# Kernel tuning notes

Measured on AMD Instinct MI355X. Metric: run time of the kernel, lower is better.

The kernel has to match this reference:

```python
import jax, jax.numpy as jnp
import numpy as np

IN_FEATURES = 1024
OUT_FEATURES = 512
TAU_U = 20.0
DT = 1.0


def setup_inputs() -> dict:
    key = jax.random.key(0)
    k_x, k_w = jax.random.split(key)
    B, T = 32, 1024
    x = jax.random.normal(k_x, (B, T, IN_FEATURES), dtype=jnp.float32)
    # uniform(-sqrt(1/in), sqrt(1/in)) as in reset_parameters
    bound = float(np.sqrt(1.0 / IN_FEATURES))
    weight = jax.random.uniform(k_w, (OUT_FEATURES, IN_FEATURES), dtype=jnp.float32,
                                minval=-bound, maxval=bound)
    bias = jnp.zeros((OUT_FEATURES,), dtype=jnp.float32)
    # fixed tau trainer: decay = exp(-dt / tau), tau fixed at 20
    decay_u = jnp.full((OUT_FEATURES,), float(np.exp(-DT / TAU_U)), dtype=jnp.float32)
    return {"x": x, "weight": weight, "bias": bias, "decay_u": decay_u}


def reference(x, weight, bias, decay_u):
    # x: [B, T, in] -> current: [B, T, out] (one big GEMM instead of T small ones)
    current = jnp.einsum("bti,oi->bto", x, weight) + bias
    B = x.shape[0]
    u0 = jnp.zeros((B, OUT_FEATURES), dtype=x.dtype)

    drive = (1.0 - decay_u) * current          # [B, T, out]
    drive_t = jnp.swapaxes(drive, 0, 1)        # [T, B, out] for scan

    def step(u_tm1, d_t):
        u_t = decay_u * u_tm1 + d_t
        return u_t, u_t

    _, outs_t = jax.lax.scan(step, u0, drive_t)  # [T, B, out]
    outputs = jnp.swapaxes(outs_t, 0, 1)          # [B, T, out]
    # states: stack([u0, u1, ..., uT], dim=1).unsqueeze(0) -> [1, B, T+1, out]
    states = jnp.concatenate([u0[:, None, :], outputs], axis=1)[None]
    return outputs, states
```

## Files before the change

### kernel.cpp

```cpp
#include <hip/hip_runtime.h>
#include <hip/hip_bf16.h>
#include <stdint.h>

#define BATCH 32
#define SEQT  1024
#define INF   1024
#define OUTF  512
#define MROWS (BATCH * SEQT)

typedef __attribute__((ext_vector_type(8))) short short8;
typedef __attribute__((ext_vector_type(4))) short s16x4;
typedef __attribute__((ext_vector_type(4))) float f32x4;

__device__ __forceinline__ short f2bf(float f) {
    return (short)__builtin_bit_cast(unsigned short, __float2bfloat16(f));
}

__device__ __forceinline__ void gll16(const short* g, short* l) {
    __builtin_amdgcn_global_load_lds(
        (const __attribute__((address_space(1))) unsigned int*)g,
        (__attribute__((address_space(3))) unsigned int*)l, 16, 0, 0);
}

__global__ __launch_bounds__(256) void wcvt_kernel(
    const float* __restrict__ W, short* __restrict__ Wb) {
    const int i = (blockIdx.x * 256 + threadIdx.x) << 3;
    const f32x4 a = *(const f32x4*)&W[i];
    const f32x4 b = *(const f32x4*)&W[i + 4];
    short8 h;
#pragma unroll
    for (int q = 0; q < 4; ++q) { h[q] = f2bf(a[q]); h[4 + q] = f2bf(b[q]); }
    *(short8*)&Wb[i] = h;
}

__global__ __launch_bounds__(256) void scanx_kernel(
    const float* __restrict__ X, const float* __restrict__ decay,
    short* __restrict__ Xs, float* __restrict__ states) {
    const int gid = blockIdx.x * 256 + threadIdx.x;
    const int k4  = gid & 255;
    const int seg = (gid >> 8) & 7;
    const int b   = gid >> 11;

    const float d   = decay[0];
    const float omd = 1.0f - d;
    const float* xb = X  + (size_t)b * SEQT * INF + (k4 << 2);
    short*       ob = Xs + (size_t)b * SEQT * INF + (k4 << 2);

    if (seg == 0 && k4 < 128) {
        f32x4 z = {0.f, 0.f, 0.f, 0.f};
        *(f32x4*)&states[(size_t)b * ((SEQT + 1) * OUTF) + (k4 << 2)] = z;
    }

    f32x4 u = {0.f, 0.f, 0.f, 0.f};
    const int t0 = seg << 7;
    const int tw = (seg == 0) ? 0 : (t0 - 128);
    for (int t = tw; t < t0; t += 8) {
        f32x4 r[8];
#pragma unroll
        for (int j = 0; j < 8; ++j) r[j] = *(const f32x4*)&xb[(size_t)(t + j) * INF];
#pragma unroll
        for (int j = 0; j < 8; ++j)
#pragma unroll
            for (int q = 0; q < 4; ++q) u[q] = fmaf(d, u[q], omd * r[j][q]);
    }
    for (int t = t0; t < t0 + 128; t += 8) {
        f32x4 r[8];
#pragma unroll
        for (int j = 0; j < 8; ++j) r[j] = *(const f32x4*)&xb[(size_t)(t + j) * INF];
#pragma unroll
        for (int j = 0; j < 8; ++j) {
            s16x4 h;
#pragma unroll
            for (int q = 0; q < 4; ++q) { u[q] = fmaf(d, u[q], omd * r[j][q]); h[q] = f2bf(u[q]); }
            *(s16x4*)&ob[(size_t)(t + j) * INF] = h;
        }
    }
}

__global__ __launch_bounds__(512, 1) void gemm_bf16_kernel(
    const short* __restrict__ Xs, const short* __restrict__ Wb,
    const float* __restrict__ bias, const float* __restrict__ decay,
    float* __restrict__ outp, float* __restrict__ states, const int writeOut) {
    __shared__ short lds_s[65536];

    const int tid = threadIdx.x;
    const int bid = blockIdx.x;
    const int xcd = bid & 7;
    const int ii  = bid >> 3;
    const int mt  = (xcd << 4) + (ii >> 1);
    const int nt  = ii & 1;
    const int m0 = mt << 8;
    const int o0 = nt << 8;

    const int wv   = tid >> 6;
    const int lane = tid & 63;
    const int wr = wv >> 1;
    const int wc = wv & 1;
    const int r0 = lane & 15;
    const int lg = lane >> 4;

    const short* sA[4];
    const short* sB[4];
    int dG[4];
#pragma unroll
    for (int j = 0; j < 4; ++j) {
        const int gf  = (j << 9) + tid;
        const int row = gf >> 3;
        const int ss  = (gf & 7) ^ (row & 7);
        sA[j] = Xs + (size_t)(m0 + row) * INF + (ss << 3);
        sB[j] = Wb + (size_t)(o0 + row) * INF + (ss << 3);
        dG[j] = gf << 3;
    }

#define STAGE(BUF, KB)                                                       \
    {                                                                        \
        short* a_ = &lds_s[(BUF) << 15];                                     \
        short* b_ = a_ + 16384;                                              \
        _Pragma("unroll")                                                    \
        for (int j = 0; j < 4; ++j) gll16(sA[j] + (KB), &a_[dG[j]]);         \
        _Pragma("unroll")                                                    \
        for (int j = 0; j < 4; ++j) gll16(sB[j] + (KB), &b_[dG[j]]);         \
    }

    f32x4 acc[4][8] = {};

    STAGE(0, 0)
    __syncthreads();

    for (int kt = 0; kt < 16; ++kt) {
        if (kt < 15) STAGE((kt + 1) & 1, (kt + 1) << 6);
        const short* la = &lds_s[(kt & 1) << 15];
        const short* lb = la + 16384;
#pragma unroll
        for (int kk = 0; kk < 2; ++kk) {
            short8 av[4], bv[8];
#pragma unroll
            for (int mi = 0; mi < 4; ++mi) {
                const int row = (wr << 6) + (mi << 4) + r0;
                const int g   = (kk << 2) + lg;
                av[mi] = *(const short8*)&la[(row << 6) + ((g ^ (row & 7)) << 3)];
            }
#pragma unroll
            for (int ni = 0; ni < 8; ++ni) {
                const int row = (wc << 7) + (ni << 4) + r0;
                const int g   = (kk << 2) + lg;
                bv[ni] = *(const short8*)&lb[(row << 6) + ((g ^ (row & 7)) << 3)];
            }
            __builtin_amdgcn_s_setprio(1);
#pragma unroll
            for (int mi = 0; mi < 4; ++mi)
#pragma unroll
                for (int ni = 0; ni < 8; ++ni)
                    acc[mi][ni] = __builtin_amdgcn_mfma_f32_16x16x32_bf16(
                        av[mi], bv[ni], acc[mi][ni], 0, 0, 0);
            __builtin_amdgcn_s_setprio(0);
        }
        __syncthreads();
    }
#undef STAGE

    float* csf = (float*)lds_s;
    const float l2d = log2f(decay[0]);
    const int b = m0 >> 10;
#pragma unroll
    for (int p = 0; p < 4; ++p) {
        if (wr == p) {
#pragma unroll
            for (int ni = 0; ni < 8; ++ni) {
                const int col = (wc << 7) + (ni << 4) + r0;
#pragma unroll
                for (int mi = 0; mi < 4; ++mi) {
                    const int lr = (mi << 4) + (lg << 2);
#pragma unroll
                    for (int j = 0; j < 4; ++j)
                        csf[(lr + j) * 260 + col] = acc[mi][ni][j];
                }
            }
        }
        __syncthreads();
#pragma unroll
        for (int it = 0; it < 8; ++it) {
            const int idx = (it << 9) + tid;
            const int row = idx >> 6;
            const int c4  = idx & 63;
            f32x4 v = *(const f32x4*)&csf[row * 260 + (c4 << 2)];
            const int m = m0 + (p << 6) + row;
            const int t = m & (SEQT - 1);
            const float coef = 1.0f - exp2f(l2d * (float)(t + 1));
            const f32x4 bb = *(const f32x4*)&bias[o0 + (c4 << 2)];
#pragma unroll
            for (int q = 0; q < 4; ++q) v[q] = fmaf(bb[q], coef, v[q]);
            const size_t oaddr = (size_t)m * OUTF + o0 + (c4 << 2);
            if (writeOut) *(f32x4*)&outp[oaddr] = v;
            *(f32x4*)&states[oaddr + (size_t)(b + 1) * OUTF] = v;
        }
        if (p < 3) __syncthreads();
    }
}

__global__ __launch_bounds__(256) void copy_out_kernel(
    float* __restrict__ outp, const float* __restrict__ states) {
    const size_t total = (size_t)MROWS * OUTF / 4;
    size_t i = (size_t)blockIdx.x * 256 + threadIdx.x;
    const size_t stride = (size_t)gridDim.x * 256;
    for (; i < total; i += stride) {
        const size_t b = i >> 17;
        *(f32x4*)&outp[i << 2] = *(const f32x4*)&states[(i << 2) + (b + 1) * OUTF];
    }
}

extern "C" void kernel_launch(void* const* d_in, const int* in_sizes, int n_in,
                              void* d_out, int out_size, void* d_ws, size_t ws_size,
                              hipStream_t stream) {
    const float* x     = (const float*)d_in[0];
    const float* w     = (const float*)d_in[1];
    const float* bias  = (const float*)d_in[2];
    const float* decay = (const float*)d_in[3];

    float* outp   = (float*)d_out;
    float* states = outp + (size_t)MROWS * OUTF;

    const size_t xs_shorts = (size_t)MROWS * INF;
    const size_t need = (xs_shorts + (size_t)OUTF * INF) * 2;
    const bool primary = (ws_size >= need);

    short* xs  = primary ? (short*)d_ws : (short*)outp;
    short* wbf = primary ? ((short*)d_ws + xs_shorts) : (short*)d_ws;

    wcvt_kernel<<<dim3((OUTF * INF) / (256 * 8)), dim3(256), 0, stream>>>(w, wbf);
    scanx_kernel<<<dim3(256), dim3(256), 0, stream>>>(x, decay, xs, states);
    gemm_bf16_kernel<<<dim3(256), dim3(512), 0, stream>>>(
        xs, wbf, bias, decay, outp, states, primary ? 1 : 0);
    if (!primary)
        copy_out_kernel<<<dim3(2048), dim3(256), 0, stream>>>(outp, states);
}
```

Before: 108.6 us.

## Double-buffer input scan loads and halve per-thread width to double threads

The input-side decay scan now has each thread handle two features instead of four, which doubles the grid from 256 to 512 blocks. Each thread loads 16 timesteps at a time into two register buffers that alternate, so the loads for the next burst are issued while the current burst is scanned. Scheduling barriers keep the compiler from interleaving the two phases. The aim is more memory-level parallelism in this bandwidth-bound pre-pass, at the cost of narrower 8-byte loads and 4-byte stores and more registers per thread.

```diff
diff --git a/kernel.cpp b/kernel.cpp
--- a/kernel.cpp
+++ b/kernel.cpp
@@ -9,7 +9,8 @@
 #define MROWS (BATCH * SEQT)
 
 typedef __attribute__((ext_vector_type(8))) short short8;
-typedef __attribute__((ext_vector_type(4))) short s16x4;
+typedef __attribute__((ext_vector_type(2))) short s16x2;
+typedef __attribute__((ext_vector_type(2))) float f32x2;
 typedef __attribute__((ext_vector_type(4))) float f32x4;
 
 __device__ __forceinline__ short f2bf(float f) {
@@ -37,44 +38,60 @@
     const float* __restrict__ X, const float* __restrict__ decay,
     short* __restrict__ Xs, float* __restrict__ states) {
     const int gid = blockIdx.x * 256 + threadIdx.x;
-    const int k4  = gid & 255;
-    const int seg = (gid >> 8) & 7;
-    const int b   = gid >> 11;
+    const int k2  = gid & 511;
+    const int seg = (gid >> 9) & 7;
+    const int b   = gid >> 12;
 
     const float d   = decay[0];
     const float omd = 1.0f - d;
-    const float* xb = X  + (size_t)b * SEQT * INF + (k4 << 2);
-    short*       ob = Xs + (size_t)b * SEQT * INF + (k4 << 2);
-
-    if (seg == 0 && k4 < 128) {
-        f32x4 z = {0.f, 0.f, 0.f, 0.f};
-        *(f32x4*)&states[(size_t)b * ((SEQT + 1) * OUTF) + (k4 << 2)] = z;
-    }
-
-    f32x4 u = {0.f, 0.f, 0.f, 0.f};
+    const float* xb = X  + (size_t)b * SEQT * INF + (k2 << 1);
+    short*       ob = Xs + (size_t)b * SEQT * INF + (k2 << 1);
+
+    if (seg == 0 && k2 < 256) {
+        f32x2 z = {0.f, 0.f};
+        *(f32x2*)&states[(size_t)b * ((SEQT + 1) * OUTF) + (k2 << 1)] = z;
+    }
+
+    float u0 = 0.f, u1 = 0.f;
     const int t0 = seg << 7;
     const int tw = (seg == 0) ? 0 : (t0 - 128);
-    for (int t = tw; t < t0; t += 8) {
-        f32x4 r[8];
-#pragma unroll
-        for (int j = 0; j < 8; ++j) r[j] = *(const f32x4*)&xb[(size_t)(t + j) * INF];
-#pragma unroll
-        for (int j = 0; j < 8; ++j)
-#pragma unroll
-            for (int q = 0; q < 4; ++q) u[q] = fmaf(d, u[q], omd * r[j][q]);
-    }
-    for (int t = t0; t < t0 + 128; t += 8) {
-        f32x4 r[8];
-#pragma unroll
-        for (int j = 0; j < 8; ++j) r[j] = *(const f32x4*)&xb[(size_t)(t + j) * INF];
-#pragma unroll
-        for (int j = 0; j < 8; ++j) {
-            s16x4 h;
-#pragma unroll
-            for (int q = 0; q < 4; ++q) { u[q] = fmaf(d, u[q], omd * r[j][q]); h[q] = f2bf(u[q]); }
-            *(s16x4*)&ob[(size_t)(t + j) * INF] = h;
-        }
-    }
+    const int nbursts = (t0 - tw + 128) >> 4;
+
+    f32x2 bufA[16], bufB[16];
+
+#define LOADB(BUF, T)                                                        \
+    _Pragma("unroll")                                                        \
+    for (int j = 0; j < 16; ++j) BUF[j] = *(const f32x2*)&xb[(size_t)((T) + j) * INF];
+
+#define PROCB(BUF, T)                                                        \
+    {                                                                        \
+        const bool mn_ = (T) >= t0;                                          \
+        _Pragma("unroll")                                                    \
+        for (int j = 0; j < 16; ++j) {                                       \
+            u0 = fmaf(d, u0, omd * BUF[j][0]);                               \
+            u1 = fmaf(d, u1, omd * BUF[j][1]);                               \
+            if (mn_) {                                                       \
+                s16x2 h; h[0] = f2bf(u0); h[1] = f2bf(u1);                   \
+                *(s16x2*)&ob[(size_t)((T) + j) * INF] = h;                   \
+            }                                                                \
+        }                                                                    \
+    }
+
+    int t = tw;
+    LOADB(bufA, t)
+    for (int burst = 0; burst < nbursts; burst += 2) {
+        if (burst + 1 < nbursts) { LOADB(bufB, t + 16) }
+        __builtin_amdgcn_sched_barrier(0);
+        PROCB(bufA, t)
+        t += 16;
+        if (burst + 1 >= nbursts) break;
+        if (burst + 2 < nbursts) { LOADB(bufA, t + 16) }
+        __builtin_amdgcn_sched_barrier(0);
+        PROCB(bufB, t)
+        t += 16;
+    }
+#undef LOADB
+#undef PROCB
 }
 
 __global__ __launch_bounds__(512, 1) void gemm_bf16_kernel(
@@ -228,7 +245,7 @@
     short* wbf = primary ? ((short*)d_ws + xs_shorts) : (short*)d_ws;
 
     wcvt_kernel<<<dim3((OUTF * INF) / (256 * 8)), dim3(256), 0, stream>>>(w, wbf);
-    scanx_kernel<<<dim3(256), dim3(256), 0, stream>>>(x, decay, xs, states);
+    scanx_kernel<<<dim3(512), dim3(256), 0, stream>>>(x, decay, xs, states);
     gemm_bf16_kernel<<<dim3(256), dim3(512), 0, stream>>>(
         xs, wbf, bias, decay, outp, states, primary ? 1 : 0);
     if (!primary)
```

After: 109.9 us. About the same (+1.2%).

## Restructure input scan to stage X tiles through LDS with wider blocks

Applied to the files above, without the earlier changes.

The prefix scan over X now uses 512-thread blocks, with each block covering 256 time steps and half of the input features. Tiles of 64 rows are staged into LDS with global_load_lds, and each thread scans a single column from LDS, writing bf16 scalar stores. The warm-up prefix drops from 128 to 128 steps over a longer segment, so redundant warm-up reads shrink relative to useful work. This trades vectorized register loads for asynchronous LDS staging, at the cost of two barriers per tile, 2-byte scalar stores, and limited loads in flight per tile.

```diff
diff --git a/kernel.cpp b/kernel.cpp
--- a/kernel.cpp
+++ b/kernel.cpp
@@ -9,14 +9,13 @@
 #define MROWS (BATCH * SEQT)
 
 typedef __attribute__((ext_vector_type(8))) short short8;
-typedef __attribute__((ext_vector_type(4))) short s16x4;
 typedef __attribute__((ext_vector_type(4))) float f32x4;
 
 __device__ __forceinline__ short f2bf(float f) {
     return (short)__builtin_bit_cast(unsigned short, __float2bfloat16(f));
 }
 
-__device__ __forceinline__ void gll16(const short* g, short* l) {
+__device__ __forceinline__ void gll16(const void* g, void* l) {
     __builtin_amdgcn_global_load_lds(
         (const __attribute__((address_space(1))) unsigned int*)g,
         (__attribute__((address_space(3))) unsigned int*)l, 16, 0, 0);
@@ -33,47 +32,58 @@
     *(short8*)&Wb[i] = h;
 }
 
-__global__ __launch_bounds__(256) void scanx_kernel(
+__global__ __launch_bounds__(512) void scanx_kernel(
     const float* __restrict__ X, const float* __restrict__ decay,
     short* __restrict__ Xs, float* __restrict__ states) {
-    const int gid = blockIdx.x * 256 + threadIdx.x;
-    const int k4  = gid & 255;
-    const int seg = (gid >> 8) & 7;
-    const int b   = gid >> 11;
+    __shared__ float tile[64][516];
+
+    const int bid = blockIdx.x;
+    const int kh  = bid & 1;
+    const int seg = (bid >> 1) & 3;
+    const int b   = bid >> 3;
+    const int tid = threadIdx.x;
+    const int wv  = tid >> 6;
+    const int ln  = tid & 63;
 
     const float d   = decay[0];
     const float omd = 1.0f - d;
-    const float* xb = X  + (size_t)b * SEQT * INF + (k4 << 2);
-    short*       ob = Xs + (size_t)b * SEQT * INF + (k4 << 2);
-
-    if (seg == 0 && k4 < 128) {
+
+    const int t0 = seg << 8;
+    const int p0 = (seg == 0) ? 2 : 0;
+
+    if (seg == 0 && kh == 0 && tid < 128) {
         f32x4 z = {0.f, 0.f, 0.f, 0.f};
-        *(f32x4*)&states[(size_t)b * ((SEQT + 1) * OUTF) + (k4 << 2)] = z;
-    }
-
-    f32x4 u = {0.f, 0.f, 0.f, 0.f};
-    const int t0 = seg << 7;
-    const int tw = (seg == 0) ? 0 : (t0 - 128);
-    for (int t = tw; t < t0; t += 8) {
-        f32x4 r[8];
-#pragma unroll
-        for (int j = 0; j < 8; ++j) r[j] = *(const f32x4*)&xb[(size_t)(t + j) * INF];
-#pragma unroll
-        for (int j = 0; j < 8; ++j)
-#pragma unroll
-            for (int q = 0; q < 4; ++q) u[q] = fmaf(d, u[q], omd * r[j][q]);
-    }
-    for (int t = t0; t < t0 + 128; t += 8) {
-        f32x4 r[8];
-#pragma unroll
-        for (int j = 0; j < 8; ++j) r[j] = *(const f32x4*)&xb[(size_t)(t + j) * INF];
-#pragma unroll
-        for (int j = 0; j < 8; ++j) {
-            s16x4 h;
-#pragma unroll
-            for (int q = 0; q < 4; ++q) { u[q] = fmaf(d, u[q], omd * r[j][q]); h[q] = f2bf(u[q]); }
-            *(s16x4*)&ob[(size_t)(t + j) * INF] = h;
-        }
+        *(f32x4*)&states[(size_t)b * ((SEQT + 1) * OUTF) + (tid << 2)] = z;
+    }
+
+    const float* xbase = X + ((size_t)b * SEQT) * INF + (kh << 9);
+    short*       obase = Xs + ((size_t)b * SEQT) * INF + (kh << 9) + tid;
+
+    float u = 0.f;
+    for (int p = p0; p < 6; ++p) {
+        const int tr = t0 - 128 + (p << 6);
+#pragma unroll
+        for (int rr = 0; rr < 8; ++rr) {
+            const int r = (rr << 3) + wv;
+            const float* src = xbase + (size_t)(tr + r) * INF + (ln << 2);
+            gll16(src,       &tile[r][ln << 2]);
+            gll16(src + 256, &tile[r][256 + (ln << 2)]);
+        }
+        __syncthreads();
+
+        if (p >= 2) {
+            short* op = obase + (size_t)tr * INF;
+#pragma unroll 8
+            for (int r = 0; r < 64; ++r) {
+                u = fmaf(d, u, omd * tile[r][tid]);
+                op[(size_t)r * INF] = f2bf(u);
+            }
+        } else {
+#pragma unroll 8
+            for (int r = 0; r < 64; ++r)
+                u = fmaf(d, u, omd * tile[r][tid]);
+        }
+        __syncthreads();
     }
 }
 
@@ -228,7 +238,7 @@
     short* wbf = primary ? ((short*)d_ws + xs_shorts) : (short*)d_ws;
 
     wcvt_kernel<<<dim3((OUTF * INF) / (256 * 8)), dim3(256), 0, stream>>>(w, wbf);
-    scanx_kernel<<<dim3(256), dim3(256), 0, stream>>>(x, decay, xs, states);
+    scanx_kernel<<<dim3(256), dim3(512), 0, stream>>>(x, decay, xs, states);
     gemm_bf16_kernel<<<dim3(256), dim3(512), 0, stream>>>(
         xs, wbf, bias, decay, outp, states, primary ? 1 : 0);
     if (!primary)
```

Result: faster. 106.0 us (-2.4%).
